# Performance work log

Hardware: AMD Instinct MI355X
Metric: run time of the kernel (lower is better)

## Reference

```python
import jax, jax.numpy as jnp
import numpy as np

N = 100000   # vertices
T = 128      # temporal depth
E = 1600000  # edges (avg degree 16)
K = 9        # conv kernel size
PAD = 4      # 'same' padding -> T preserved
L = 3        # number of layers


def setup_inputs() -> dict:
    key = jax.random.key(0)
    ks = jax.random.split(key, 6)
    x = jax.random.normal(ks[0], (N, T), dtype=jnp.float32)
    edge_index = jax.random.randint(ks[1], (2, E), 0, N, dtype=jnp.int32)
    conv_w = jax.random.normal(ks[2], (L, 1, 1, K), dtype=jnp.float32) * (1.0 / np.sqrt(K))
    conv_b = jax.random.normal(ks[3], (L, 1), dtype=jnp.float32) * 0.1
    W_out = jax.random.normal(ks[4], (3, N), dtype=jnp.float32) * (1.0 / np.sqrt(N))
    b_out = jax.random.normal(ks[5], (3,), dtype=jnp.float32) * 0.1
    return {"x": x, "edge_index": edge_index, "conv_w": conv_w,
            "conv_b": conv_b, "W_out": W_out, "b_out": b_out}


def _conv1d(x, w, b):
    # x: [N, T], w: [1, 1, K] (OIH), b: [1]; torch Conv1d = cross-correlation.
    y = jax.lax.conv_general_dilated(
        x[:, None, :], w, window_strides=(1,), padding=[(PAD, PAD)],
        dimension_numbers=("NCH", "OIH", "NCH"))
    return y[:, 0, :] + b  # [N, T]


def reference(x, edge_index, conv_w, conv_b, W_out, b_out):
    # add_self_loops: append (i, i) for every node
    loop = jnp.arange(N, dtype=edge_index.dtype)
    src = jnp.concatenate([edge_index[0], loop])  # message sources
    dst = jnp.concatenate([edge_index[1], loop])  # aggregation targets
    # in-degree counts (>=1 due to self loops) for mean aggregation
    cnt = jax.ops.segment_sum(jnp.ones(src.shape, jnp.float32), dst,
                              num_segments=N)[:, None]  # [N, 1]
    for i in range(L):
        h = _conv1d(x, conv_w[i], conv_b[i])                    # [N, T]
        s = jax.ops.segment_sum(h[src], dst, num_segments=N)    # scatter-sum of gathered msgs
        x = jax.nn.relu(s / cnt)                                # mean aggr + relu
    x = x.reshape(-1, N)            # [T, N] (row-major view like torch .view)
    return x @ W_out.T + b_out      # [T, 3]
```

## Files before the change

kernel.cpp:

```cpp
#include <hip/hip_runtime.h>

#define NN 100000
#define TT 128
#define EE 1600000
#define KK 9
#define NSPLIT 16

#define BSH 9
#define BMASK 511
#define NBUCK 196
#define BCAP 10240
#define EPB 4096
#define BINB 391
#define CVTB 3125

typedef _Float16 f16;
typedef __attribute__((ext_vector_type(2))) _Float16 f16x2;
typedef __attribute__((ext_vector_type(4))) _Float16 f16x4;
typedef __attribute__((ext_vector_type(8))) _Float16 f16x8;

union HU8 { f16x8 h; int4 i; };

__global__ __launch_bounds__(1024)
void bin_cvt_kernel(const int* __restrict__ ei, int* __restrict__ gcursor,
                    unsigned int* __restrict__ binned,
                    const float4* __restrict__ x, f16x4* __restrict__ x16,
                    float* __restrict__ out) {
    __shared__ int hist[NBUCK];
    __shared__ int gbase[NBUCK];
    int tid = threadIdx.x;

    if (blockIdx.x >= BINB + CVTB) {
        if (tid < TT * 3) out[tid] = 0.0f;
        return;
    }
    if (blockIdx.x >= BINB) {
        int i = (blockIdx.x - BINB) * 1024 + tid;
        float4 v = x[i];
        f16x4 o;
        o.x = (f16)v.x; o.y = (f16)v.y; o.z = (f16)v.z; o.w = (f16)v.w;
        x16[i] = o;
        return;
    }

    if (tid < NBUCK) hist[tid] = 0;
    __syncthreads();
    int base = blockIdx.x * EPB;
    unsigned int val[4];
    short bkt[4];
    short rank[4];
#pragma unroll
    for (int k = 0; k < 4; k++) {
        int e = base + k * 1024 + tid;
        bkt[k] = -1;
        if (e < EE) {
            int s = ei[e];
            int d = ei[EE + e];
            bkt[k] = (short)(d >> BSH);
            val[k] = ((unsigned int)(d & BMASK) << 20) | (unsigned int)s;
            rank[k] = (short)atomicAdd(&hist[bkt[k]], 1);
        }
    }
    __syncthreads();
    if (tid < NBUCK) gbase[tid] = hist[tid] ? atomicAdd(&gcursor[tid], hist[tid]) : 0;
    __syncthreads();
#pragma unroll
    for (int k = 0; k < 4; k++) {
        if (bkt[k] >= 0)
            binned[(size_t)bkt[k] * BCAP + gbase[bkt[k]] + (int)rank[k]] = val[k];
    }
}

__global__ __launch_bounds__(1024)
void bucket_csr_kernel(const unsigned int* __restrict__ binned,
                       const int* __restrict__ gcursor,
                       int* __restrict__ offsets,
                       float* __restrict__ inv_cnt,
                       int* __restrict__ col) {
    __shared__ int hist[512];
    __shared__ int cur[512];
    __shared__ int smB[256];
    __shared__ int sc[512];
    int b = blockIdx.x;
    int tid = threadIdx.x;

    if (tid < 256) smB[tid] = (tid < NBUCK) ? gcursor[tid] : 0;
    __syncthreads();
    for (int off = 1; off < 256; off <<= 1) {
        int v = 0;
        if (tid < 256 && tid >= off) v = smB[tid - off];
        __syncthreads();
        if (tid < 256) smB[tid] += v;
        __syncthreads();
    }
    int bucket_base = (b == 0) ? 0 : smB[b - 1];
    if (b == 0 && tid == 0) offsets[NN] = EE;

    int cnt = gcursor[b];
    const unsigned int* ePtr = binned + (size_t)b * BCAP;
    if (tid < 512) hist[tid] = 0;
    __syncthreads();
    for (int j = tid; j < cnt; j += 1024)
        atomicAdd(&hist[ePtr[j] >> 20], 1);
    __syncthreads();
    int d = (tid < 512) ? hist[tid] : 0;
    if (tid < 512) sc[tid] = d;
    __syncthreads();
    for (int off = 1; off < 512; off <<= 1) {
        int v = 0;
        if (tid < 512 && tid >= off) v = sc[tid - off];
        __syncthreads();
        if (tid < 512) sc[tid] += v;
        __syncthreads();
    }
    if (tid < 512) {
        int node = (b << BSH) + tid;
        int pos = bucket_base + sc[tid] - d;
        if (node < NN) {
            offsets[node] = pos;
            inv_cnt[node] = 1.0f / (1.0f + (float)d);
            cur[tid] = pos;
        }
    }
    __syncthreads();
    for (int j = tid; j < cnt; j += 1024) {
        unsigned int v = ePtr[j];
        int pos = atomicAdd(&cur[v >> 20], 1);
        col[pos] = (int)(v & 0xFFFFF);
    }
}

__device__ __forceinline__ void gather_conv_node(
    const f16x8* __restrict__ xin, const int* __restrict__ offsets,
    const int* __restrict__ col, const float* __restrict__ inv_cnt,
    const float* wr, float bb, int node, int lane, int q, int p, float* s)
{
    int lo = offsets[node], hi = offsets[node + 1];
    int cnt = hi - lo;
    int my_col = (lane < cnt) ? col[lo + lane] : 0;
    int jn = cnt < 64 ? cnt : 64;

    const f16 z = (f16)0;
    f16x8 acc0 = {z, z, z, z, z, z, z, z};
    f16x8 acc1 = {z, z, z, z, z, z, z, z};

    int j = 0;
    for (; j + 7 < jn; j += 8) {
        int c0 = __shfl(my_col, j + q);
        int c1 = __shfl(my_col, j + 4 + q);
        f16x8 v0 = xin[(c0 << 4) | p];
        f16x8 v1 = xin[(c1 << 4) | p];
        acc0 += v0;
        acc1 += v1;
    }
    for (; j + 3 < jn; j += 4) {
        int c = __shfl(my_col, j + q);
        acc0 += xin[(c << 4) | p];
    }
    if (j < jn) {
        int rem = jn - j;
        int c = __shfl(my_col, j + (q < rem ? q : 0));
        f16x8 v = xin[(c << 4) | p];
        if (q < rem) acc1 += v;
    }
    for (int k = 64; k < cnt; k++) {
        int c = col[lo + k];
        f16x8 v = xin[(c << 4) | p];
        if (q == 0) acc0 += v;
    }
    acc0 += acc1;

    {
        HU8 u; u.h = acc0;
        int4 o;
        o.x = __shfl_xor(u.i.x, 16); o.y = __shfl_xor(u.i.y, 16);
        o.z = __shfl_xor(u.i.z, 16); o.w = __shfl_xor(u.i.w, 16);
        HU8 w2; w2.i = o;
        acc0 += w2.h;
        u.h = acc0;
        o.x = __shfl_xor(u.i.x, 32); o.y = __shfl_xor(u.i.y, 32);
        o.z = __shfl_xor(u.i.z, 32); o.w = __shfl_xor(u.i.w, 32);
        w2.i = o;
        acc0 += w2.h;
    }

    f16x8 sv = xin[(node << 4) | p];
    float A[16];
    A[4]  = (float)acc0[0] + (float)sv[0];
    A[5]  = (float)acc0[1] + (float)sv[1];
    A[6]  = (float)acc0[2] + (float)sv[2];
    A[7]  = (float)acc0[3] + (float)sv[3];
    A[8]  = (float)acc0[4] + (float)sv[4];
    A[9]  = (float)acc0[5] + (float)sv[5];
    A[10] = (float)acc0[6] + (float)sv[6];
    A[11] = (float)acc0[7] + (float)sv[7];
#pragma unroll
    for (int i = 0; i < 4; i++) {
        A[i]      = __shfl_up(A[8 + i], 1, 16);
        A[12 + i] = __shfl_down(A[4 + i], 1, 16);
    }
    if (p == 0)  { A[0] = 0.0f; A[1] = 0.0f; A[2] = 0.0f; A[3] = 0.0f; }
    if (p == 15) { A[12] = 0.0f; A[13] = 0.0f; A[14] = 0.0f; A[15] = 0.0f; }

    float ic = inv_cnt[node];
#pragma unroll
    for (int i = 0; i < 8; i++) {
        float t = 0.0f;
#pragma unroll
        for (int k = 0; k < KK; k++) t += wr[k] * A[i + k];
        s[i] = fmaxf(t * ic + bb, 0.0f);
    }
}

__global__ void fused_layer_kernel(const f16x8* __restrict__ xin,
                                   const int* __restrict__ offsets,
                                   const int* __restrict__ col,
                                   const float* __restrict__ inv_cnt,
                                   const float* __restrict__ w9,
                                   const float* __restrict__ bptr,
                                   f16x8* __restrict__ yout) {
    int tid = threadIdx.x;
    int lane = tid & 63;
    int q = lane >> 4;
    int p = lane & 15;
    int node = blockIdx.x * 4 + (tid >> 6);
    float wr[KK];
#pragma unroll
    for (int k = 0; k < KK; k++) wr[k] = w9[k];
    float s[8];
    gather_conv_node(xin, offsets, col, inv_cnt, wr, bptr[0], node, lane, q, p, s);
    if (q == 0) {
        f16x8 o;
#pragma unroll
        for (int i = 0; i < 8; i++) o[i] = (f16)s[i];
        yout[(node << 4) | p] = o;
    }
}

__global__ void out_kernel(const f16* __restrict__ y3, const float* __restrict__ Wout,
                           const float* __restrict__ bout, float* __restrict__ out) {
    int t = blockIdx.x;
    int sp = blockIdx.y;
    int tid = threadIdx.x;
    const int per = NN / NSPLIT;
    int lo = sp * per;
    int hi = lo + per;
    float a0 = 0.0f, a1 = 0.0f, a2 = 0.0f;
    for (int n = lo + tid * 2; n < hi; n += 512) {
        f16x2 v2 = *(const f16x2*)(y3 + (size_t)t * NN + n);
        float vx = (float)v2.x, vy = (float)v2.y;
        float2 wA = *(const float2*)(Wout + n);
        float2 wB = *(const float2*)(Wout + NN + n);
        float2 wC = *(const float2*)(Wout + 2 * NN + n);
        a0 += vx * wA.x + vy * wA.y;
        a1 += vx * wB.x + vy * wB.y;
        a2 += vx * wC.x + vy * wC.y;
    }
    for (int o = 32; o > 0; o >>= 1) {
        a0 += __shfl_down(a0, o);
        a1 += __shfl_down(a1, o);
        a2 += __shfl_down(a2, o);
    }
    __shared__ float red[4][3];
    int wave = tid >> 6;
    if ((tid & 63) == 0) {
        red[wave][0] = a0;
        red[wave][1] = a1;
        red[wave][2] = a2;
    }
    __syncthreads();
    if (tid == 0) {
        float r0 = red[0][0] + red[1][0] + red[2][0] + red[3][0];
        float r1 = red[0][1] + red[1][1] + red[2][1] + red[3][1];
        float r2 = red[0][2] + red[1][2] + red[2][2] + red[3][2];
        if (sp == 0) {
            r0 += bout[0];
            r1 += bout[1];
            r2 += bout[2];
        }
        atomicAdd(&out[t * 3 + 0], r0);
        atomicAdd(&out[t * 3 + 1], r1);
        atomicAdd(&out[t * 3 + 2], r2);
    }
}

extern "C" void kernel_launch(void* const* d_in, const int* in_sizes, int n_in,
                              void* d_out, int out_size, void* d_ws, size_t ws_size,
                              hipStream_t stream) {
    const float4* x    = (const float4*)d_in[0];
    const int*    ei   = (const int*)d_in[1];
    const float*  cw   = (const float*)d_in[2];
    const float*  cb   = (const float*)d_in[3];
    const float*  Wout = (const float*)d_in[4];
    const float*  bout = (const float*)d_in[5];
    float* out = (float*)d_out;

    char* ws = (char*)d_ws;
    size_t off = 0;
    auto alloc = [&](size_t bytes) -> void* {
        void* p = ws + off;
        off += (bytes + 255) & ~(size_t)255;
        return p;
    };
    f16x8*        x16     = (f16x8*)alloc((size_t)NN * TT * 2);
    f16x8*        yA      = (f16x8*)alloc((size_t)NN * TT * 2);
    f16x8*        yB      = (f16x8*)alloc((size_t)NN * TT * 2);
    unsigned int* binned  = (unsigned int*)alloc((size_t)NBUCK * BCAP * 4);
    int*          gcursor = (int*)alloc((size_t)NBUCK * 4);
    int*          offsets = (int*)alloc((size_t)(NN + 1) * 4);
    float*        inv_cnt = (float*)alloc((size_t)NN * 4);
    int*          col     = (int*)alloc((size_t)EE * 4);

    hipMemsetAsync(gcursor, 0, (size_t)NBUCK * 4, stream);
    bin_cvt_kernel<<<BINB + CVTB + 1, 1024, 0, stream>>>(ei, gcursor, binned,
                                                         x, (f16x4*)x16, out);
    bucket_csr_kernel<<<NBUCK, 1024, 0, stream>>>(binned, gcursor, offsets, inv_cnt, col);

    fused_layer_kernel<<<NN / 4, 256, 0, stream>>>(x16, offsets, col, inv_cnt,
                                                   cw + 0 * KK, cb + 0, yA);
    fused_layer_kernel<<<NN / 4, 256, 0, stream>>>(yA, offsets, col, inv_cnt,
                                                   cw + 1 * KK, cb + 1, yB);
    fused_layer_kernel<<<NN / 4, 256, 0, stream>>>(yB, offsets, col, inv_cnt,
                                                   cw + 2 * KK, cb + 2, yA);

    out_kernel<<<dim3(TT, NSPLIT), 256, 0, stream>>>((const f16*)yA, Wout, bout, out);
}
```

Baseline: 333.5 us.

## Fuse final GCN layer with output projection using per-node atomic reduction

The third layer's gather-conv now computes each node's 128 outputs and immediately dots them with the matching slice of W_out under the flattened [T,N] view. The partial sums are reduced within each 16-lane group and added to the output with atomics. This removes the fp16 write of the final activation and the separate out_kernel that read it back. The bias is now written into the output at init time instead of being added at the end. The cost is about 25k blocks times 3 atomics onto only 384 output addresses, which may cause atomic contention.

```diff
diff --git a/kernel.cpp b/kernel.cpp
--- a/kernel.cpp
+++ b/kernel.cpp
@@ -4,7 +4,6 @@
 #define TT 128
 #define EE 1600000
 #define KK 9
-#define NSPLIT 16
 
 #define BSH 9
 #define BMASK 511
@@ -15,7 +14,6 @@
 #define CVTB 3125
 
 typedef _Float16 f16;
-typedef __attribute__((ext_vector_type(2))) _Float16 f16x2;
 typedef __attribute__((ext_vector_type(4))) _Float16 f16x4;
 typedef __attribute__((ext_vector_type(8))) _Float16 f16x8;
 
@@ -25,13 +23,13 @@
 void bin_cvt_kernel(const int* __restrict__ ei, int* __restrict__ gcursor,
                     unsigned int* __restrict__ binned,
                     const float4* __restrict__ x, f16x4* __restrict__ x16,
-                    float* __restrict__ out) {
+                    const float* __restrict__ bout, float* __restrict__ out) {
     __shared__ int hist[NBUCK];
     __shared__ int gbase[NBUCK];
     int tid = threadIdx.x;
 
     if (blockIdx.x >= BINB + CVTB) {
-        if (tid < TT * 3) out[tid] = 0.0f;
+        if (tid < TT * 3) out[tid] = bout[tid - (tid / 3) * 3];
         return;
     }
     if (blockIdx.x >= BINB) {
@@ -237,50 +235,49 @@
     }
 }
 
-__global__ void out_kernel(const f16* __restrict__ y3, const float* __restrict__ Wout,
-                           const float* __restrict__ bout, float* __restrict__ out) {
-    int t = blockIdx.x;
-    int sp = blockIdx.y;
+__global__ void layer3_out_kernel(const f16x8* __restrict__ xin,
+                                  const int* __restrict__ offsets,
+                                  const int* __restrict__ col,
+                                  const float* __restrict__ inv_cnt,
+                                  const float* __restrict__ w9,
+                                  const float* __restrict__ bptr,
+                                  const float* __restrict__ Wout,
+                                  float* __restrict__ out) {
     int tid = threadIdx.x;
-    const int per = NN / NSPLIT;
-    int lo = sp * per;
-    int hi = lo + per;
-    float a0 = 0.0f, a1 = 0.0f, a2 = 0.0f;
-    for (int n = lo + tid * 2; n < hi; n += 512) {
-        f16x2 v2 = *(const f16x2*)(y3 + (size_t)t * NN + n);
-        float vx = (float)v2.x, vy = (float)v2.y;
-        float2 wA = *(const float2*)(Wout + n);
-        float2 wB = *(const float2*)(Wout + NN + n);
-        float2 wC = *(const float2*)(Wout + 2 * NN + n);
-        a0 += vx * wA.x + vy * wA.y;
-        a1 += vx * wB.x + vy * wB.y;
-        a2 += vx * wC.x + vy * wC.y;
-    }
-    for (int o = 32; o > 0; o >>= 1) {
-        a0 += __shfl_down(a0, o);
-        a1 += __shfl_down(a1, o);
-        a2 += __shfl_down(a2, o);
-    }
-    __shared__ float red[4][3];
-    int wave = tid >> 6;
-    if ((tid & 63) == 0) {
-        red[wave][0] = a0;
-        red[wave][1] = a1;
-        red[wave][2] = a2;
-    }
-    __syncthreads();
-    if (tid == 0) {
-        float r0 = red[0][0] + red[1][0] + red[2][0] + red[3][0];
-        float r1 = red[0][1] + red[1][1] + red[2][1] + red[3][1];
-        float r2 = red[0][2] + red[1][2] + red[2][2] + red[3][2];
-        if (sp == 0) {
-            r0 += bout[0];
-            r1 += bout[1];
-            r2 += bout[2];
+    int lane = tid & 63;
+    int q = lane >> 4;
+    int p = lane & 15;
+    int node = blockIdx.x * 4 + (tid >> 6);
+    float wr[KK];
+#pragma unroll
+    for (int k = 0; k < KK; k++) wr[k] = w9[k];
+    float s[8];
+    gather_conv_node(xin, offsets, col, inv_cnt, wr, bptr[0], node, lane, q, p, s);
+
+    int f0 = node * TT;
+    int t0 = f0 / NN;
+    int r0 = f0 - t0 * NN;
+    if (r0 + TT <= NN) {
+        if (q < 3) {
+            const float4* Wrow = (const float4*)(Wout + q * NN + r0 + 8 * p);
+            float4 w0 = Wrow[0];
+            float4 w1 = Wrow[1];
+            float a = s[0] * w0.x + s[1] * w0.y + s[2] * w0.z + s[3] * w0.w
+                    + s[4] * w1.x + s[5] * w1.y + s[6] * w1.z + s[7] * w1.w;
+            for (int o = 8; o > 0; o >>= 1) a += __shfl_down(a, o, 16);
+            if (p == 0) atomicAdd(&out[t0 * 3 + q], a);
         }
-        atomicAdd(&out[t * 3 + 0], r0);
-        atomicAdd(&out[t * 3 + 1], r1);
-        atomicAdd(&out[t * 3 + 2], r2);
+    } else if (q == 0) {
+#pragma unroll
+        for (int i = 0; i < 8; i++) {
+            int f = f0 + 8 * p + i;
+            int t = f / NN;
+            int nw = f - t * NN;
+            float v = s[i];
+            atomicAdd(&out[t * 3 + 0], v * Wout[nw]);
+            atomicAdd(&out[t * 3 + 1], v * Wout[NN + nw]);
+            atomicAdd(&out[t * 3 + 2], v * Wout[2 * NN + nw]);
+        }
     }
 }
 
@@ -313,15 +310,13 @@
 
     hipMemsetAsync(gcursor, 0, (size_t)NBUCK * 4, stream);
     bin_cvt_kernel<<<BINB + CVTB + 1, 1024, 0, stream>>>(ei, gcursor, binned,
-                                                         x, (f16x4*)x16, out);
+                                                         x, (f16x4*)x16, bout, out);
     bucket_csr_kernel<<<NBUCK, 1024, 0, stream>>>(binned, gcursor, offsets, inv_cnt, col);
 
     fused_layer_kernel<<<NN / 4, 256, 0, stream>>>(x16, offsets, col, inv_cnt,
                                                    cw + 0 * KK, cb + 0, yA);
     fused_layer_kernel<<<NN / 4, 256, 0, stream>>>(yA, offsets, col, inv_cnt,
                                                    cw + 1 * KK, cb + 1, yB);
-    fused_layer_kernel<<<NN / 4, 256, 0, stream>>>(yB, offsets, col, inv_cnt,
-                                                   cw + 2 * KK, cb + 2, yA);
-
-    out_kernel<<<dim3(TT, NSPLIT), 256, 0, stream>>>((const f16*)yA, Wout, bout, out);
-}
+    layer3_out_kernel<<<NN / 4, 256, 0, stream>>>(yB, offsets, col, inv_cnt,
+                                                  cw + 2 * KK, cb + 2, Wout, out);
+}
```

After: 688.6 us. 2.06x slower.

## Restructure output projection into partial-sum and reduce kernels; enlarge layer blocks

Applied to the files above, without the earlier changes.

The output projection is split into a partial kernel, where each block covers a node slice across 8 time steps so its Wout slice is reused from cache, and a small reduce kernel that adds the bias. This removes the atomics and the zeroing of the output buffer. The fused layer kernel now runs 1024-thread blocks holding 16 nodes each instead of 4. It adds one kernel launch and a partial buffer, and the larger blocks may change occupancy.

```diff
diff --git a/kernel.cpp b/kernel.cpp
--- a/kernel.cpp
+++ b/kernel.cpp
@@ -4,7 +4,6 @@
 #define TT 128
 #define EE 1600000
 #define KK 9
-#define NSPLIT 16
 
 #define BSH 9
 #define BMASK 511
@@ -14,6 +13,10 @@
 #define BINB 391
 #define CVTB 3125
 
+#define OSLICE 1568
+#define ONS 64
+#define OTG 16
+
 typedef _Float16 f16;
 typedef __attribute__((ext_vector_type(2))) _Float16 f16x2;
 typedef __attribute__((ext_vector_type(4))) _Float16 f16x4;
@@ -24,16 +27,11 @@
 __global__ __launch_bounds__(1024)
 void bin_cvt_kernel(const int* __restrict__ ei, int* __restrict__ gcursor,
                     unsigned int* __restrict__ binned,
-                    const float4* __restrict__ x, f16x4* __restrict__ x16,
-                    float* __restrict__ out) {
+                    const float4* __restrict__ x, f16x4* __restrict__ x16) {
     __shared__ int hist[NBUCK];
     __shared__ int gbase[NBUCK];
     int tid = threadIdx.x;
 
-    if (blockIdx.x >= BINB + CVTB) {
-        if (tid < TT * 3) out[tid] = 0.0f;
-        return;
-    }
     if (blockIdx.x >= BINB) {
         int i = (blockIdx.x - BINB) * 1024 + tid;
         float4 v = x[i];
@@ -212,18 +210,19 @@
     }
 }
 
-__global__ void fused_layer_kernel(const f16x8* __restrict__ xin,
-                                   const int* __restrict__ offsets,
-                                   const int* __restrict__ col,
-                                   const float* __restrict__ inv_cnt,
-                                   const float* __restrict__ w9,
-                                   const float* __restrict__ bptr,
-                                   f16x8* __restrict__ yout) {
+__global__ __launch_bounds__(1024)
+void fused_layer_kernel(const f16x8* __restrict__ xin,
+                        const int* __restrict__ offsets,
+                        const int* __restrict__ col,
+                        const float* __restrict__ inv_cnt,
+                        const float* __restrict__ w9,
+                        const float* __restrict__ bptr,
+                        f16x8* __restrict__ yout) {
     int tid = threadIdx.x;
     int lane = tid & 63;
     int q = lane >> 4;
     int p = lane & 15;
-    int node = blockIdx.x * 4 + (tid >> 6);
+    int node = blockIdx.x * 16 + (tid >> 6);
     float wr[KK];
 #pragma unroll
     for (int k = 0; k < KK; k++) wr[k] = w9[k];
@@ -237,50 +236,70 @@
     }
 }
 
-__global__ void out_kernel(const f16* __restrict__ y3, const float* __restrict__ Wout,
-                           const float* __restrict__ bout, float* __restrict__ out) {
+__global__ void out_partial_kernel(const f16* __restrict__ y3,
+                                   const float* __restrict__ Wout,
+                                   float* __restrict__ partial) {
+    __shared__ float red[4][3];
+    int sp = blockIdx.x;
+    int tg = blockIdx.y;
+    int tid = threadIdx.x;
+    int lane = tid & 63;
+    int wave = tid >> 6;
+    int n0 = sp * OSLICE;
+    int n1 = n0 + OSLICE;
+    if (n1 > NN) n1 = NN;
+    for (int t = tg * 8; t < tg * 8 + 8; t++) {
+        const f16* yrow = y3 + (size_t)t * NN;
+        float a0 = 0.0f, a1 = 0.0f, a2 = 0.0f;
+        for (int n = n0 + tid * 2; n < n1; n += 512) {
+            f16x2 v = *(const f16x2*)(yrow + n);
+            float vx = (float)v.x, vy = (float)v.y;
+            float2 wA = *(const float2*)(Wout + n);
+            float2 wB = *(const float2*)(Wout + NN + n);
+            float2 wC = *(const float2*)(Wout + 2 * NN + n);
+            a0 += vx * wA.x + vy * wA.y;
+            a1 += vx * wB.x + vy * wB.y;
+            a2 += vx * wC.x + vy * wC.y;
+        }
+        for (int o = 32; o > 0; o >>= 1) {
+            a0 += __shfl_down(a0, o);
+            a1 += __shfl_down(a1, o);
+            a2 += __shfl_down(a2, o);
+        }
+        if (lane == 0) {
+            red[wave][0] = a0;
+            red[wave][1] = a1;
+            red[wave][2] = a2;
+        }
+        __syncthreads();
+        if (tid == 0) {
+            int idx = (t * ONS + sp) * 3;
+            partial[idx + 0] = red[0][0] + red[1][0] + red[2][0] + red[3][0];
+            partial[idx + 1] = red[0][1] + red[1][1] + red[2][1] + red[3][1];
+            partial[idx + 2] = red[0][2] + red[1][2] + red[2][2] + red[3][2];
+        }
+        __syncthreads();
+    }
+}
+
+__global__ void out_reduce_kernel(const float* __restrict__ partial,
+                                  const float* __restrict__ bout,
+                                  float* __restrict__ out) {
     int t = blockIdx.x;
-    int sp = blockIdx.y;
-    int tid = threadIdx.x;
-    const int per = NN / NSPLIT;
-    int lo = sp * per;
-    int hi = lo + per;
-    float a0 = 0.0f, a1 = 0.0f, a2 = 0.0f;
-    for (int n = lo + tid * 2; n < hi; n += 512) {
-        f16x2 v2 = *(const f16x2*)(y3 + (size_t)t * NN + n);
-        float vx = (float)v2.x, vy = (float)v2.y;
-        float2 wA = *(const float2*)(Wout + n);
-        float2 wB = *(const float2*)(Wout + NN + n);
-        float2 wC = *(const float2*)(Wout + 2 * NN + n);
-        a0 += vx * wA.x + vy * wA.y;
-        a1 += vx * wB.x + vy * wB.y;
-        a2 += vx * wC.x + vy * wC.y;
-    }
+    int l = threadIdx.x;
+    int idx = (t * ONS + l) * 3;
+    float a0 = partial[idx + 0];
+    float a1 = partial[idx + 1];
+    float a2 = partial[idx + 2];
     for (int o = 32; o > 0; o >>= 1) {
         a0 += __shfl_down(a0, o);
         a1 += __shfl_down(a1, o);
         a2 += __shfl_down(a2, o);
     }
-    __shared__ float red[4][3];
-    int wave = tid >> 6;
-    if ((tid & 63) == 0) {
-        red[wave][0] = a0;
-        red[wave][1] = a1;
-        red[wave][2] = a2;
-    }
-    __syncthreads();
-    if (tid == 0) {
-        float r0 = red[0][0] + red[1][0] + red[2][0] + red[3][0];
-        float r1 = red[0][1] + red[1][1] + red[2][1] + red[3][1];
-        float r2 = red[0][2] + red[1][2] + red[2][2] + red[3][2];
-        if (sp == 0) {
-            r0 += bout[0];
-            r1 += bout[1];
-            r2 += bout[2];
-        }
-        atomicAdd(&out[t * 3 + 0], r0);
-        atomicAdd(&out[t * 3 + 1], r1);
-        atomicAdd(&out[t * 3 + 2], r2);
+    if (l == 0) {
+        out[t * 3 + 0] = bout[0] + a0;
+        out[t * 3 + 1] = bout[1] + a1;
+        out[t * 3 + 2] = bout[2] + a2;
     }
 }
 
@@ -310,18 +329,19 @@
     int*          offsets = (int*)alloc((size_t)(NN + 1) * 4);
     float*        inv_cnt = (float*)alloc((size_t)NN * 4);
     int*          col     = (int*)alloc((size_t)EE * 4);
+    float*        partial = (float*)alloc((size_t)TT * ONS * 3 * 4);
 
     hipMemsetAsync(gcursor, 0, (size_t)NBUCK * 4, stream);
-    bin_cvt_kernel<<<BINB + CVTB + 1, 1024, 0, stream>>>(ei, gcursor, binned,
-                                                         x, (f16x4*)x16, out);
+    bin_cvt_kernel<<<BINB + CVTB, 1024, 0, stream>>>(ei, gcursor, binned, x, (f16x4*)x16);
     bucket_csr_kernel<<<NBUCK, 1024, 0, stream>>>(binned, gcursor, offsets, inv_cnt, col);
 
-    fused_layer_kernel<<<NN / 4, 256, 0, stream>>>(x16, offsets, col, inv_cnt,
-                                                   cw + 0 * KK, cb + 0, yA);
-    fused_layer_kernel<<<NN / 4, 256, 0, stream>>>(yA, offsets, col, inv_cnt,
-                                                   cw + 1 * KK, cb + 1, yB);
-    fused_layer_kernel<<<NN / 4, 256, 0, stream>>>(yB, offsets, col, inv_cnt,
-                                                   cw + 2 * KK, cb + 2, yA);
-
-    out_kernel<<<dim3(TT, NSPLIT), 256, 0, stream>>>((const f16*)yA, Wout, bout, out);
-}
+    fused_layer_kernel<<<NN / 16, 1024, 0, stream>>>(x16, offsets, col, inv_cnt,
+                                                     cw + 0 * KK, cb + 0, yA);
+    fused_layer_kernel<<<NN / 16, 1024, 0, stream>>>(yA, offsets, col, inv_cnt,
+                                                     cw + 1 * KK, cb + 1, yB);
+    fused_layer_kernel<<<NN / 16, 1024, 0, stream>>>(yB, offsets, col, inv_cnt,
+                                                     cw + 2 * KK, cb + 2, yA);
+
+    out_partial_kernel<<<dim3(ONS, OTG), 256, 0, stream>>>((const f16*)yA, Wout, partial);
+    out_reduce_kernel<<<TT, 64, 0, stream>>>(partial, bout, out);
+}
```

Result: slower. 352.5 us (+5.7%).
